# Optimization experiments

Hardware: AMD Instinct MI355X
Metric: run time of the kernel (lower is better)

## Reference

```python
import jax, jax.numpy as jnp
import numpy as np

VOCAB, SEQ, D_EMB, D_HID, BATCH = 50257, 256, 256, 512, 16

def setup_inputs() -> dict:
    key = jax.random.key(0)
    ks = jax.random.split(key, 8)
    s_e = 1.0 / np.sqrt(D_EMB)
    s_h = 1.0 / np.sqrt(D_HID)
    return {
        "idx": jax.random.randint(ks[0], (BATCH, SEQ), 0, VOCAB),
        "E":  jax.random.normal(ks[1], (VOCAB, D_EMB), jnp.float32) * 0.02,
        "Wi": jax.random.normal(ks[2], (D_EMB, 4 * D_HID), jnp.float32) * s_e,  # input kernel (no bias in flax LSTMCell)
        "Wh": jax.random.normal(ks[3], (D_HID, 4 * D_HID), jnp.float32) * s_h,  # recurrent kernel
        "bh": jnp.zeros((4 * D_HID,), jnp.float32),                              # recurrent bias
        "Wo": jax.random.normal(ks[4], (D_HID, VOCAB), jnp.float32) * s_h,
        "bo": jnp.zeros((VOCAB,), jnp.float32),
    }

def reference(idx, E, Wi, Wh, bh, Wo, bo):
    B, S = idx.shape
    H = Wh.shape[0]
    x = E[idx]                                   # [B, S, D] embedding gather
    # precompute input contribution for all timesteps: [S, B, 4H]
    xz = jnp.einsum('bsd,dg->sbg', x, Wi)

    def step(carry, xz_t):
        h, c = carry
        z = xz_t + h @ Wh + bh                   # [B, 4H]
        i, f, g, o = jnp.split(z, 4, axis=-1)    # flax gate order: i, f, g, o
        i = jax.nn.sigmoid(i)
        f = jax.nn.sigmoid(f)
        g = jnp.tanh(g)
        o = jax.nn.sigmoid(o)
        c = f * c + i * g
        h = o * jnp.tanh(c)
        return (h, c), h

    h0 = jnp.zeros((B, H), x.dtype)
    c0 = jnp.zeros((B, H), x.dtype)
    _, hs = jax.lax.scan(step, (h0, c0), xz)     # hs: [S, B, H]
    hs = jnp.transpose(hs, (1, 0, 2))            # [B, S, H]
    logits = hs @ Wo + bo                        # [B, S, V]
    return logits
```

## Files before the change

### kernel.cpp

```cpp
#include <hip/hip_runtime.h>
#include <cstdint>


typedef __attribute__((ext_vector_type(8))) short short8;
typedef __attribute__((ext_vector_type(4))) float f32x4;
typedef __attribute__((ext_vector_type(4))) unsigned int u32x4;
typedef __attribute__((ext_vector_type(4))) unsigned short ush4;

#define DEVFN static __device__ __forceinline__

DEVFN unsigned short f2bf(float f) {
    unsigned int u = __float_as_uint(f);
    return (unsigned short)((u + 0x7FFFu + ((u >> 16) & 1u)) >> 16);
}
DEVFN float bf2f(unsigned short h) { return __uint_as_float(((unsigned int)h) << 16); }
DEVFN float sigm(float x) { return 1.0f / (1.0f + __expf(-x)); }
DEVFN float tanh_fast(float x) {
    float e = __expf(-2.0f * fabsf(x));
    float t = (1.0f - e) / (1.0f + e);
    return copysignf(t, x);
}
DEVFN f32x4 fzero() { f32x4 v = {0.f, 0.f, 0.f, 0.f}; return v; }

DEVFN uint32_t ld_flag_mall(const uint32_t* p) {
    uint32_t v;
    asm volatile("global_load_dword %0, %1, off sc0 sc1\n\ts_waitcnt vmcnt(0)"
                 : "=v"(v) : "v"(p) : "memory");
    return v;
}
DEVFN void st_flag_mall(uint32_t* p, uint32_t v) {
    asm volatile("global_store_dword %0, %1, off sc0 sc1" :: "v"(p), "v"(v) : "memory");
}
DEVFN void aload16(u32x4& d, const void* p) {
    asm volatile("global_load_dwordx4 %0, %1, off sc0 sc1" : "=v"(d) : "v"(p));
}

__global__ __launch_bounds__(256) void k0_wot(const float* __restrict__ Wo,
                                              uint32_t* __restrict__ WoTP) {
    __shared__ float tile[32][33];
    const int bx = blockIdx.x;
    const int cb = bx >> 4;
    const int kb = bx & 15;
    const int c0 = cb * 32, k0 = kb * 32;
    const int j = threadIdx.x & 31;
    const int i0 = threadIdx.x >> 5;
    for (int ii = i0; ii < 32; ii += 8) {
        const int c = c0 + j;
        tile[ii][j] = (c < 50257) ? Wo[(size_t)(k0 + ii) * 50257 + c] : 0.0f;
    }
    __syncthreads();
    for (int ii = i0; ii < 32; ii += 8) {
        const float v = tile[j][ii];
        const unsigned short hi = f2bf(v);
        const unsigned short lo = f2bf(v - bf2f(hi));
        WoTP[(size_t)(c0 + ii) * 512 + k0 + j] = (((unsigned int)hi) << 16) | lo;
    }
}

__global__ __launch_bounds__(256) void k0b_whlo(const float* __restrict__ Wh,
                                                uint32_t* __restrict__ WLO) {
    const int tid = blockIdx.x * 256 + threadIdx.x;
    const int lane = tid & 63;
    const int q    = (tid >> 6) & 15;
    const int nt   = (tid >> 10) & 1;
    const int vp   = tid >> 11;
    const int cc   = lane & 15;
    const int gcol = (cc >> 2) * 512 + vp * 8 + nt * 4 + (cc & 3);
    const int kbase = q * 32 + (lane >> 4) * 8;
    u32x4 o;
#pragma unroll
    for (int p = 0; p < 4; ++p) {
        unsigned int pair = 0;
#pragma unroll
        for (int e = 0; e < 2; ++e) {
            const int k = kbase + p * 2 + e;
            const float w = Wh[(size_t)k * 2048 + gcol];
            const unsigned short hi = f2bf(w);
            const unsigned short lo = f2bf(w - bf2f(hi));
            pair |= ((unsigned int)lo) << (e * 16);
        }
        o[p] = pair;
    }
    *(u32x4*)(WLO + (size_t)tid * 4) = o;
}

__global__ __launch_bounds__(256) void k1_xz(const int* __restrict__ idx,
                                             const float* __restrict__ E,
                                             const float* __restrict__ Wi,
                                             unsigned short* __restrict__ xzH) {
    __shared__ float xs[16][256];
    const int s = blockIdx.x;
    const int t = threadIdx.x;
#pragma unroll
    for (int b = 0; b < 16; ++b) {
        const int row = idx[b * 256 + s];
        xs[b][t] = E[(size_t)row * 256 + t];
    }
    __syncthreads();
    for (int half = 0; half < 2; ++half) {
        const int g0 = half * 1024 + t * 4;
        f32x4 acc[16];
#pragma unroll
        for (int b = 0; b < 16; ++b) acc[b] = fzero();
        for (int d = 0; d < 256; ++d) {
            const f32x4 w = *(const f32x4*)&Wi[(size_t)d * 2048 + g0];
#pragma unroll
            for (int b = 0; b < 16; ++b) {
                const float xv = xs[b][d];
                acc[b] += xv * w;
            }
        }
#pragma unroll
        for (int b = 0; b < 16; ++b) {
            ush4 o;
#pragma unroll
            for (int jj = 0; jj < 4; ++jj) o[jj] = f2bf(acc[b][jj]);
            *(ush4*)&xzH[((size_t)s * 16 + b) * 2048 + g0] = o;
        }
    }
}

__global__ __launch_bounds__(256, 1) void k23(const float* __restrict__ Wh,
                                              const float* __restrict__ bh,
                                              const unsigned short* __restrict__ xzH,
                                              const short8* __restrict__ WLO8,
                                              uint32_t* __restrict__ hsP,
                                              const uint32_t* __restrict__ zeroh,
                                              uint32_t* __restrict__ ep,
                                              uint32_t* __restrict__ epC,
                                              const uint32_t* __restrict__ WoTP,
                                              const float* __restrict__ bo,
                                              float* __restrict__ out) {
    __shared__ __align__(16) char smem[131072];
    __shared__ unsigned int sEp;

    const int tid = threadIdx.x;

    if (blockIdx.x < 16) {
        const int blk = blockIdx.x;

        for (int vs = 0; vs < 4; ++vs) {
            const int vp_s = blk * 4 + vs;
            const int l = tid >> 3, seg = tid & 7;
            const int cc = l & 15, nt0 = l >> 4;
            const int gcol = (cc >> 2) * 512 + vp_s * 8 + nt0 * 4 + (cc & 3);
            for (int k8 = seg * 64; k8 < seg * 64 + 64; k8 += 8) {
                short8 v;
#pragma unroll
                for (int i = 0; i < 8; ++i)
                    v[i] = (short)f2bf(Wh[(size_t)(k8 + i) * 2048 + gcol]);
                const int slot = (k8 >> 3) ^ (l & 7);
                *(short8*)(smem + vs * 32768 + l * 1024 + slot * 16) = v;
            }
        }
        if (tid == 0) sEp = 0;
        __syncthreads();

        const int w = tid >> 6;
        const int lane = tid & 63;
        const int vp = blk * 4 + w;
        unsigned short* whhW = (unsigned short*)(smem + w * 32768);
        const int c = lane & 15;
        const int qtr = lane >> 4;

        int gc[2];
        float bh_v[2];
#pragma unroll
        for (int nt = 0; nt < 2; ++nt) {
            gc[nt] = (c >> 2) * 512 + vp * 8 + nt * 4 + (c & 3);
            bh_v[nt] = bh[gc[nt]];
        }
        float cst[2][4];
#pragma unroll
        for (int nt = 0; nt < 2; ++nt)
#pragma unroll
            for (int r = 0; r < 4; ++r) cst[nt][r] = 0.0f;

        float xzv[2][4];
#pragma unroll
        for (int nt = 0; nt < 2; ++nt)
#pragma unroll
            for (int r = 0; r < 4; ++r)
                xzv[nt][r] = bf2f(xzH[(size_t)(qtr * 4 + r) * 2048 + gc[nt]]);

        short8 bz = {0, 0, 0, 0, 0, 0, 0, 0};
        f32x4 bd0 = fzero(), bd1 = fzero();

        for (int t = 0; t < 256; ++t) {
            if (t > 0) {
                const uint32_t tgt = 16u * (uint32_t)t;
                if (w == 0) {
                    while (true) {
                        const uint32_t v = ld_flag_mall(ep);
                        if (v >= tgt) break;
#pragma unroll
                        for (int i = 0; i < 2; ++i) {
                            bd0 = __builtin_amdgcn_mfma_f32_16x16x32_bf16(bz, bz, bd0, 0, 0, 0);
                            bd1 = __builtin_amdgcn_mfma_f32_16x16x32_bf16(bz, bz, bd1, 0, 0, 0);
                        }
                    }
                    if (lane == 0) {
                        __hip_atomic_store(&sEp, (unsigned)t, __ATOMIC_RELAXED,
                                           __HIP_MEMORY_SCOPE_WORKGROUP);
                        if (blk == 0) st_flag_mall(epC, (uint32_t)t);
                    }
                } else {
                    while (__hip_atomic_load(&sEp, __ATOMIC_RELAXED,
                                             __HIP_MEMORY_SCOPE_WORKGROUP) < (unsigned)t) {}
                }
                __builtin_amdgcn_sched_barrier(0);
            }

            const uint32_t* hbase = (t == 0)
                ? (zeroh + (size_t)c * 512)
                : (hsP + ((size_t)(t - 1) * 16 + c) * 512);

            f32x4 acc[2][2];
#pragma unroll
            for (int nt = 0; nt < 2; ++nt) { acc[nt][0] = fzero(); acc[nt][1] = fzero(); }

#pragma unroll
            for (int q = 0; q < 16; ++q) {
                const int kb = q * 32 + qtr * 8;
                const unsigned long long* hb64 = (const unsigned long long*)(hbase + kb);
                unsigned long long d[4];
#pragma unroll
                for (int i = 0; i < 4; ++i)
                    d[i] = __hip_atomic_load(hb64 + i, __ATOMIC_RELAXED,
                                             __HIP_MEMORY_SCOPE_AGENT);
                short8 ahi, alo;
#pragma unroll
                for (int i = 0; i < 4; ++i) {
                    const uint32_t wlo32 = (uint32_t)d[i];
                    const uint32_t whi32 = (uint32_t)(d[i] >> 32);
                    ahi[2 * i]     = (short)(wlo32 >> 16); alo[2 * i]     = (short)(wlo32 & 0xffffu);
                    ahi[2 * i + 1] = (short)(whi32 >> 16); alo[2 * i + 1] = (short)(whi32 & 0xffffu);
                }
#pragma unroll
                for (int nt = 0; nt < 2; ++nt) {
                    const int l = nt * 16 + c;
                    const short8 bhi = *(const short8*)((const char*)whhW + l * 1024 +
                                                        (((q * 4 + qtr) ^ (l & 7)) << 4));
                    const short8 blo = WLO8[(((size_t)vp * 2 + nt) * 16 + q) * 64 + lane];
                    f32x4 a = acc[nt][q & 1];
                    a = __builtin_amdgcn_mfma_f32_16x16x32_bf16(ahi, bhi, a, 0, 0, 0);
                    a = __builtin_amdgcn_mfma_f32_16x16x32_bf16(ahi, blo, a, 0, 0, 0);
                    a = __builtin_amdgcn_mfma_f32_16x16x32_bf16(alo, bhi, a, 0, 0, 0);
                    acc[nt][q & 1] = a;
                }
            }

#pragma unroll
            for (int nt = 0; nt < 2; ++nt) {
                f32x4 z4 = acc[nt][0] + acc[nt][1];
#pragma unroll
                for (int r = 0; r < 4; ++r) z4[r] += xzv[nt][r] + bh_v[nt];
#pragma unroll
                for (int r = 0; r < 4; ++r) {
                    const int sb = (lane & 0x33);
                    const float zi = __shfl(z4[r], sb);
                    const float zf = __shfl(z4[r], sb | 4);
                    const float zg = __shfl(z4[r], sb | 8);
                    const float zo = __shfl(z4[r], sb | 12);
                    const float iv = sigm(zi), fv = sigm(zf);
                    const float gv = tanh_fast(zg), ov = sigm(zo);
                    const float cv = fv * cst[nt][r] + iv * gv;
                    cst[nt][r] = cv;
                    const float hv = ov * tanh_fast(cv);
                    if ((c >> 2) == 0) {
                        const unsigned short hi = f2bf(hv);
                        const unsigned short lo = f2bf(hv - bf2f(hi));
                        const uint32_t packed = (((uint32_t)hi) << 16) | lo;
                        __hip_atomic_store(
                            &hsP[((size_t)t * 16 + qtr * 4 + r) * 512 + vp * 8 + nt * 4 + c],
                            packed, __ATOMIC_RELAXED, __HIP_MEMORY_SCOPE_AGENT);
                    }
                }
            }

            asm volatile("s_waitcnt vmcnt(0)" ::: "memory");
            __syncthreads();
            if (tid == 0)
                __hip_atomic_fetch_add(ep, 1u, __ATOMIC_RELAXED, __HIP_MEMORY_SCOPE_AGENT);

            if (t < 255) {
#pragma unroll
                for (int nt = 0; nt < 2; ++nt)
#pragma unroll
                    for (int r = 0; r < 4; ++r)
                        xzv[nt][r] = bf2f(xzH[((size_t)(t + 1) * 16 + qtr * 4 + r) * 2048 + gc[nt]]);
            }
        }

        if (blk == 0 && tid == 0) {
            while (ld_flag_mall(ep) < 4096u) {}
            st_flag_mall(epC, 256u);
        }
        asm volatile("" :: "v"(bd0), "v"(bd1));
    } else {
        unsigned short (*Ah)[64] = (unsigned short(*)[64])(smem);
        unsigned short (*Al)[64] = (unsigned short(*)[64])(smem + 16384);
        unsigned short (*Bh)[64] = (unsigned short(*)[64])(smem + 32768);
        unsigned short (*Bl)[64] = (unsigned short(*)[64])(smem + 49152);

        const int cid = blockIdx.x - 16;
        const int lane = tid & 63;
        const int wv = tid >> 6;
        const int wr = wv >> 1, wc = wv & 1;
        const int srow = tid >> 1, shalf = tid & 1;

        short8 bz = {0, 0, 0, 0, 0, 0, 0, 0};
        f32x4 bd0 = fzero(), bd1 = fzero(), bd2 = fzero(), bd3 = fzero();

        for (int s0 = 0; s0 < 32; ++s0) {
            const unsigned need = (unsigned)(s0 * 8 + 8);
            while (true) {
                const uint32_t f = ld_flag_mall(epC);
                if (f >= need) break;
#pragma unroll
                for (int i = 0; i < 8; ++i) {
                    bd0 = __builtin_amdgcn_mfma_f32_16x16x32_bf16(bz, bz, bd0, 0, 0, 0);
                    bd1 = __builtin_amdgcn_mfma_f32_16x16x32_bf16(bz, bz, bd1, 0, 0, 0);
                    bd2 = __builtin_amdgcn_mfma_f32_16x16x32_bf16(bz, bz, bd2, 0, 0, 0);
                    bd3 = __builtin_amdgcn_mfma_f32_16x16x32_bf16(bz, bz, bd3, 0, 0, 0);
                }
            }

            for (int vi = 0; vi < 2; ++vi) {
                const int v = cid + vi * 240;
                if (v >= 393) break;

                f32x4 acc[4][4];
#pragma unroll
                for (int i = 0; i < 4; ++i)
#pragma unroll
                    for (int j = 0; j < 4; ++j) acc[i][j] = fzero();

                for (int kb = 0; kb < 8; ++kb) {
                    __syncthreads();
                    const uint32_t* sa = hsP + (size_t)(s0 * 128 + srow) * 512 + kb * 64 + shalf * 32;
                    const uint32_t* sbp = WoTP + (size_t)(v * 128 + srow) * 512 + kb * 64 + shalf * 32;
                    u32x4 av[8], bv[8];
#pragma unroll
                    for (int g = 0; g < 4; ++g) {
                        aload16(av[2 * g], sa + g * 8);
                        aload16(av[2 * g + 1], sa + g * 8 + 4);
                    }
#pragma unroll
                    for (int g = 0; g < 4; ++g) {
                        bv[2 * g]     = *(const u32x4*)(sbp + g * 8);
                        bv[2 * g + 1] = *(const u32x4*)(sbp + g * 8 + 4);
                    }
                    asm volatile("s_waitcnt vmcnt(0)" ::: "memory");
                    __builtin_amdgcn_sched_barrier(0);
#pragma unroll
                    for (int g = 0; g < 4; ++g) {
                        short8 hi, lo;
#pragma unroll
                        for (int i = 0; i < 4; ++i) {
                            hi[i]     = (short)(av[2 * g][i] >> 16);
                            lo[i]     = (short)(av[2 * g][i] & 0xffffu);
                            hi[4 + i] = (short)(av[2 * g + 1][i] >> 16);
                            lo[4 + i] = (short)(av[2 * g + 1][i] & 0xffffu);
                        }
                        const int sw = ((shalf * 4 + g) ^ (srow & 7)) << 4;
                        *(short8*)((char*)Ah + srow * 128 + sw) = hi;
                        *(short8*)((char*)Al + srow * 128 + sw) = lo;
                    }
#pragma unroll
                    for (int g = 0; g < 4; ++g) {
                        short8 hi, lo;
#pragma unroll
                        for (int i = 0; i < 4; ++i) {
                            hi[i]     = (short)(bv[2 * g][i] >> 16);
                            lo[i]     = (short)(bv[2 * g][i] & 0xffffu);
                            hi[4 + i] = (short)(bv[2 * g + 1][i] >> 16);
                            lo[4 + i] = (short)(bv[2 * g + 1][i] & 0xffffu);
                        }
                        const int sw = ((shalf * 4 + g) ^ (srow & 7)) << 4;
                        *(short8*)((char*)Bh + srow * 128 + sw) = hi;
                        *(short8*)((char*)Bl + srow * 128 + sw) = lo;
                    }
                    __syncthreads();

#pragma unroll
                    for (int q = 0; q < 2; ++q) {
                        short8 afh[4], afl[4], bfh[4], bfl[4];
#pragma unroll
                        for (int mi = 0; mi < 4; ++mi) {
                            const int r = wr * 64 + mi * 16 + (lane & 15);
                            const int sw = ((q * 4 + (lane >> 4)) ^ (r & 7)) << 4;
                            afh[mi] = *(const short8*)((const char*)Ah + r * 128 + sw);
                            afl[mi] = *(const short8*)((const char*)Al + r * 128 + sw);
                        }
#pragma unroll
                        for (int nj = 0; nj < 4; ++nj) {
                            const int r = wc * 64 + nj * 16 + (lane & 15);
                            const int sw = ((q * 4 + (lane >> 4)) ^ (r & 7)) << 4;
                            bfh[nj] = *(const short8*)((const char*)Bh + r * 128 + sw);
                            bfl[nj] = *(const short8*)((const char*)Bl + r * 128 + sw);
                        }
#pragma unroll
                        for (int mi = 0; mi < 4; ++mi)
#pragma unroll
                            for (int nj = 0; nj < 4; ++nj) {
                                f32x4 a = acc[mi][nj];
                                a = __builtin_amdgcn_mfma_f32_16x16x32_bf16(afh[mi], bfh[nj], a, 0, 0, 0);
                                a = __builtin_amdgcn_mfma_f32_16x16x32_bf16(afh[mi], bfl[nj], a, 0, 0, 0);
                                a = __builtin_amdgcn_mfma_f32_16x16x32_bf16(afl[mi], bfh[nj], a, 0, 0, 0);
                                acc[mi][nj] = a;
                            }
                    }
                }

#pragma unroll
                for (int nj = 0; nj < 4; ++nj) {
                    const int colg = v * 128 + wc * 64 + nj * 16 + (lane & 15);
                    if (colg < 50257) {
                        const float bov = bo[colg];
#pragma unroll
                        for (int mi = 0; mi < 4; ++mi)
#pragma unroll
                            for (int r = 0; r < 4; ++r) {
                                const int tr = wr * 64 + mi * 16 + (lane >> 4) * 4 + r;
                                const int ss = s0 * 8 + (tr >> 4);
                                const int bb = tr & 15;
                                out[((size_t)bb * 256 + ss) * 50257 + colg] = acc[mi][nj][r] + bov;
                            }
                    }
                }
            }
        }
        asm volatile("" :: "v"(bd0), "v"(bd1), "v"(bd2), "v"(bd3));
    }
}

#define XZH_OFF   0ull
#define HSP_OFF   16777216ull
#define ZEROH_OFF 25165824ull
#define FLG_OFF   25198592ull
#define WLO_OFF   25198848ull
#define WOT_OFF   27296000ull

extern "C" void kernel_launch(void* const* d_in, const int* in_sizes, int n_in,
                              void* d_out, int out_size, void* d_ws, size_t ws_size,
                              hipStream_t stream) {
    (void)in_sizes; (void)n_in; (void)out_size; (void)ws_size;
    const int*   idx = (const int*)  d_in[0];
    const float* E   = (const float*)d_in[1];
    const float* Wi  = (const float*)d_in[2];
    const float* Wh  = (const float*)d_in[3];
    const float* bh  = (const float*)d_in[4];
    const float* Wo  = (const float*)d_in[5];
    const float* bo  = (const float*)d_in[6];
    float* out = (float*)d_out;
    char* ws = (char*)d_ws;

    unsigned short* xzH   = (unsigned short*)(ws + XZH_OFF);
    uint32_t*       hsP   = (uint32_t*)      (ws + HSP_OFF);
    uint32_t*       zeroh = (uint32_t*)      (ws + ZEROH_OFF);
    uint32_t*       ep    = (uint32_t*)      (ws + FLG_OFF);
    uint32_t*       epC   = (uint32_t*)      (ws + FLG_OFF + 128);
    uint32_t*       WLO   = (uint32_t*)      (ws + WLO_OFF);
    uint32_t*       WoTP  = (uint32_t*)      (ws + WOT_OFF);

    hipMemsetAsync(ws + ZEROH_OFF, 0, 33024, stream);

    hipLaunchKernelGGL(k0_wot,   dim3(25152), dim3(256), 0, stream, Wo, WoTP);
    hipLaunchKernelGGL(k0b_whlo, dim3(512),   dim3(256), 0, stream, Wh, WLO);
    hipLaunchKernelGGL(k1_xz,    dim3(256),   dim3(256), 0, stream, idx, E, Wi, xzH);
    hipLaunchKernelGGL(k23,      dim3(256),   dim3(256), 0, stream,
                       Wh, bh, xzH, (const short8*)WLO, hsP, zeroh, ep, epC, WoTP, bo, out);
}
```

Baseline: 3.347 ms.

## Stage recurrent h in LDS per step and stream prepacked Wh hi fragments

Each recurrent block now cooperatively loads the previous step's packed hidden state (all 16 batch rows) into swizzled LDS with wide loads, then reads MFMA A-fragments from LDS instead of every wave issuing atomic 64-bit global loads. Wh hi bf16 fragments are precomputed by a prep kernel and read from global alongside the lo fragments, which frees LDS for h and removes the in-kernel Wh conversion. The per-block spin is simplified so all waves poll the global flag, replacing the wave-0 plus LDS-flag scheme, with a __syncthreads per step added. This trades per-step global atomic traffic for a block barrier and extra global reads of Wh hi.

New measurement: 3.578 ms. +6.9%, slower.

```diff
diff --git a/kernel.cpp b/kernel.cpp
--- a/kernel.cpp
+++ b/kernel.cpp
@@ -57,8 +57,9 @@
     }
 }
 
-__global__ __launch_bounds__(256) void k0b_whlo(const float* __restrict__ Wh,
-                                                uint32_t* __restrict__ WLO) {
+__global__ __launch_bounds__(256) void k0b_whfrag(const float* __restrict__ Wh,
+                                                  uint32_t* __restrict__ WHI,
+                                                  uint32_t* __restrict__ WLO) {
     const int tid = blockIdx.x * 256 + threadIdx.x;
     const int lane = tid & 63;
     const int q    = (tid >> 6) & 15;
@@ -67,21 +68,23 @@
     const int cc   = lane & 15;
     const int gcol = (cc >> 2) * 512 + vp * 8 + nt * 4 + (cc & 3);
     const int kbase = q * 32 + (lane >> 4) * 8;
-    u32x4 o;
+    u32x4 ohi, olo;
 #pragma unroll
     for (int p = 0; p < 4; ++p) {
-        unsigned int pair = 0;
+        unsigned int phi = 0, plo = 0;
 #pragma unroll
         for (int e = 0; e < 2; ++e) {
             const int k = kbase + p * 2 + e;
             const float w = Wh[(size_t)k * 2048 + gcol];
             const unsigned short hi = f2bf(w);
             const unsigned short lo = f2bf(w - bf2f(hi));
-            pair |= ((unsigned int)lo) << (e * 16);
-        }
-        o[p] = pair;
-    }
-    *(u32x4*)(WLO + (size_t)tid * 4) = o;
+            phi |= ((unsigned int)hi) << (e * 16);
+            plo |= ((unsigned int)lo) << (e * 16);
+        }
+        ohi[p] = phi; olo[p] = plo;
+    }
+    *(u32x4*)(WHI + (size_t)tid * 4) = ohi;
+    *(u32x4*)(WLO + (size_t)tid * 4) = olo;
 }
 
 __global__ __launch_bounds__(256) void k1_xz(const int* __restrict__ idx,
@@ -120,46 +123,25 @@
     }
 }
 
-__global__ __launch_bounds__(256, 1) void k23(const float* __restrict__ Wh,
-                                              const float* __restrict__ bh,
+__global__ __launch_bounds__(256, 1) void k23(const float* __restrict__ bh,
                                               const unsigned short* __restrict__ xzH,
+                                              const short8* __restrict__ WHI8,
                                               const short8* __restrict__ WLO8,
                                               uint32_t* __restrict__ hsP,
-                                              const uint32_t* __restrict__ zeroh,
                                               uint32_t* __restrict__ ep,
                                               uint32_t* __restrict__ epC,
                                               const uint32_t* __restrict__ WoTP,
                                               const float* __restrict__ bo,
                                               float* __restrict__ out) {
     __shared__ __align__(16) char smem[131072];
-    __shared__ unsigned int sEp;
 
     const int tid = threadIdx.x;
 
     if (blockIdx.x < 16) {
         const int blk = blockIdx.x;
-
-        for (int vs = 0; vs < 4; ++vs) {
-            const int vp_s = blk * 4 + vs;
-            const int l = tid >> 3, seg = tid & 7;
-            const int cc = l & 15, nt0 = l >> 4;
-            const int gcol = (cc >> 2) * 512 + vp_s * 8 + nt0 * 4 + (cc & 3);
-            for (int k8 = seg * 64; k8 < seg * 64 + 64; k8 += 8) {
-                short8 v;
-#pragma unroll
-                for (int i = 0; i < 8; ++i)
-                    v[i] = (short)f2bf(Wh[(size_t)(k8 + i) * 2048 + gcol]);
-                const int slot = (k8 >> 3) ^ (l & 7);
-                *(short8*)(smem + vs * 32768 + l * 1024 + slot * 16) = v;
-            }
-        }
-        if (tid == 0) sEp = 0;
-        __syncthreads();
-
         const int w = tid >> 6;
         const int lane = tid & 63;
         const int vp = blk * 4 + w;
-        unsigned short* whhW = (unsigned short*)(smem + w * 32768);
         const int c = lane & 15;
         const int qtr = lane >> 4;
 
@@ -189,31 +171,45 @@
         for (int t = 0; t < 256; ++t) {
             if (t > 0) {
                 const uint32_t tgt = 16u * (uint32_t)t;
-                if (w == 0) {
-                    while (true) {
-                        const uint32_t v = ld_flag_mall(ep);
-                        if (v >= tgt) break;
-#pragma unroll
-                        for (int i = 0; i < 2; ++i) {
-                            bd0 = __builtin_amdgcn_mfma_f32_16x16x32_bf16(bz, bz, bd0, 0, 0, 0);
-                            bd1 = __builtin_amdgcn_mfma_f32_16x16x32_bf16(bz, bz, bd1, 0, 0, 0);
-                        }
-                    }
-                    if (lane == 0) {
-                        __hip_atomic_store(&sEp, (unsigned)t, __ATOMIC_RELAXED,
-                                           __HIP_MEMORY_SCOPE_WORKGROUP);
-                        if (blk == 0) st_flag_mall(epC, (uint32_t)t);
-                    }
-                } else {
-                    while (__hip_atomic_load(&sEp, __ATOMIC_RELAXED,
-                                             __HIP_MEMORY_SCOPE_WORKGROUP) < (unsigned)t) {}
-                }
+                while (true) {
+                    const uint32_t v = ld_flag_mall(ep);
+                    if (v >= tgt) break;
+#pragma unroll
+                    for (int i = 0; i < 2; ++i) {
+                        bd0 = __builtin_amdgcn_mfma_f32_16x16x32_bf16(bz, bz, bd0, 0, 0, 0);
+                        bd1 = __builtin_amdgcn_mfma_f32_16x16x32_bf16(bz, bz, bd1, 0, 0, 0);
+                    }
+                }
+                if (blk == 0 && tid == 0) st_flag_mall(epC, (uint32_t)t);
                 __builtin_amdgcn_sched_barrier(0);
             }
 
-            const uint32_t* hbase = (t == 0)
-                ? (zeroh + (size_t)c * 512)
-                : (hsP + ((size_t)(t - 1) * 16 + c) * 512);
+            if (t == 0) {
+                const u32x4 z = {0u, 0u, 0u, 0u};
+#pragma unroll
+                for (int j = 0; j < 8; ++j) {
+                    const int U = j * 256 + tid;
+                    const int b = U >> 7, u = U & 127;
+                    *(u32x4*)(smem + b * 2048 + ((u ^ (b & 7)) << 4)) = z;
+                }
+            } else {
+                u32x4 gv[8];
+#pragma unroll
+                for (int j = 0; j < 8; ++j) {
+                    const int U = j * 256 + tid;
+                    const int b = U >> 7, u = U & 127;
+                    aload16(gv[j], hsP + ((size_t)(t - 1) * 16 + b) * 512 + u * 4);
+                }
+                asm volatile("s_waitcnt vmcnt(0)" ::: "memory");
+                __builtin_amdgcn_sched_barrier(0);
+#pragma unroll
+                for (int j = 0; j < 8; ++j) {
+                    const int U = j * 256 + tid;
+                    const int b = U >> 7, u = U & 127;
+                    *(u32x4*)(smem + b * 2048 + ((u ^ (b & 7)) << 4)) = gv[j];
+                }
+            }
+            __syncthreads();
 
             f32x4 acc[2][2];
 #pragma unroll
@@ -221,26 +217,18 @@
 
 #pragma unroll
             for (int q = 0; q < 16; ++q) {
-                const int kb = q * 32 + qtr * 8;
-                const unsigned long long* hb64 = (const unsigned long long*)(hbase + kb);
-                unsigned long long d[4];
-#pragma unroll
-                for (int i = 0; i < 4; ++i)
-                    d[i] = __hip_atomic_load(hb64 + i, __ATOMIC_RELAXED,
-                                             __HIP_MEMORY_SCOPE_AGENT);
+                const int u0 = q * 8 + qtr * 2;
+                const u32x4 h0 = *(const u32x4*)(smem + c * 2048 + ((u0 ^ (c & 7)) << 4));
+                const u32x4 h1 = *(const u32x4*)(smem + c * 2048 + (((u0 + 1) ^ (c & 7)) << 4));
                 short8 ahi, alo;
 #pragma unroll
                 for (int i = 0; i < 4; ++i) {
-                    const uint32_t wlo32 = (uint32_t)d[i];
-                    const uint32_t whi32 = (uint32_t)(d[i] >> 32);
-                    ahi[2 * i]     = (short)(wlo32 >> 16); alo[2 * i]     = (short)(wlo32 & 0xffffu);
-                    ahi[2 * i + 1] = (short)(whi32 >> 16); alo[2 * i + 1] = (short)(whi32 & 0xffffu);
+                    ahi[i]     = (short)(h0[i] >> 16); alo[i]     = (short)(h0[i] & 0xffffu);
+                    ahi[4 + i] = (short)(h1[i] >> 16); alo[4 + i] = (short)(h1[i] & 0xffffu);
                 }
 #pragma unroll
                 for (int nt = 0; nt < 2; ++nt) {
-                    const int l = nt * 16 + c;
-                    const short8 bhi = *(const short8*)((const char*)whhW + l * 1024 +
-                                                        (((q * 4 + qtr) ^ (l & 7)) << 4));
+                    const short8 bhi = WHI8[(((size_t)vp * 2 + nt) * 16 + q) * 64 + lane];
                     const short8 blo = WLO8[(((size_t)vp * 2 + nt) * 16 + q) * 64 + lane];
                     f32x4 a = acc[nt][q & 1];
                     a = __builtin_amdgcn_mfma_f32_16x16x32_bf16(ahi, bhi, a, 0, 0, 0);
@@ -437,10 +425,10 @@
 
 #define XZH_OFF   0ull
 #define HSP_OFF   16777216ull
-#define ZEROH_OFF 25165824ull
-#define FLG_OFF   25198592ull
-#define WLO_OFF   25198848ull
-#define WOT_OFF   27296000ull
+#define FLG_OFF   25165824ull
+#define WHI_OFF   25166080ull
+#define WLO_OFF   27263232ull
+#define WOT_OFF   29360384ull
 
 extern "C" void kernel_launch(void* const* d_in, const int* in_sizes, int n_in,
                               void* d_out, int out_size, void* d_ws, size_t ws_size,
@@ -456,19 +444,20 @@
     float* out = (float*)d_out;
     char* ws = (char*)d_ws;
 
-    unsigned short* xzH   = (unsigned short*)(ws + XZH_OFF);
-    uint32_t*       hsP   = (uint32_t*)      (ws + HSP_OFF);
-    uint32_t*       zeroh = (uint32_t*)      (ws + ZEROH_OFF);
-    uint32_t*       ep    = (uint32_t*)      (ws + FLG_OFF);
-    uint32_t*       epC   = (uint32_t*)      (ws + FLG_OFF + 128);
-    uint32_t*       WLO   = (uint32_t*)      (ws + WLO_OFF);
-    uint32_t*       WoTP  = (uint32_t*)      (ws + WOT_OFF);
-
-    hipMemsetAsync(ws + ZEROH_OFF, 0, 33024, stream);
-
-    hipLaunchKernelGGL(k0_wot,   dim3(25152), dim3(256), 0, stream, Wo, WoTP);
-    hipLaunchKernelGGL(k0b_whlo, dim3(512),   dim3(256), 0, stream, Wh, WLO);
-    hipLaunchKernelGGL(k1_xz,    dim3(256),   dim3(256), 0, stream, idx, E, Wi, xzH);
-    hipLaunchKernelGGL(k23,      dim3(256),   dim3(256), 0, stream,
-                       Wh, bh, xzH, (const short8*)WLO, hsP, zeroh, ep, epC, WoTP, bo, out);
-}
+    unsigned short* xzH  = (unsigned short*)(ws + XZH_OFF);
+    uint32_t*       hsP  = (uint32_t*)      (ws + HSP_OFF);
+    uint32_t*       ep   = (uint32_t*)      (ws + FLG_OFF);
+    uint32_t*       epC  = (uint32_t*)      (ws + FLG_OFF + 128);
+    uint32_t*       WHI  = (uint32_t*)      (ws + WHI_OFF);
+    uint32_t*       WLO  = (uint32_t*)      (ws + WLO_OFF);
+    uint32_t*       WoTP = (uint32_t*)      (ws + WOT_OFF);
+
+    hipMemsetAsync(ws + FLG_OFF, 0, 256, stream);
+
+    hipLaunchKernelGGL(k0_wot,    dim3(25152), dim3(256), 0, stream, Wo, WoTP);
+    hipLaunchKernelGGL(k0b_whfrag,dim3(512),   dim3(256), 0, stream, Wh, WHI, WLO);
+    hipLaunchKernelGGL(k1_xz,     dim3(256),   dim3(256), 0, stream, idx, E, Wi, xzH);
+    hipLaunchKernelGGL(k23,       dim3(256),   dim3(256), 0, stream,
+                       bh, xzH, (const short8*)WHI, (const short8*)WLO, hsP, ep, epC,
+                       WoTP, bo, out);
+}
```

## Use arrive/release barrier and staged vector stores for LSTM hidden state

Applied to the files above, without the earlier changes.

The grid-wide per-step barrier is restructured. Instead of wave 0 polling a shared counter and relaying through LDS, the last block to arrive publishes a release flag that every wave polls directly. The release also advances the consumer progress flag each step, which removes the final wait loop. Hidden-state outputs are staged in LDS and written as coalesced 16-byte stores instead of scattered 4-byte atomic stores. This cuts per-step barrier latency and store count, at the cost of an extra __syncthreads and more waves polling global memory.

Result: no change. 3.384 ms (+1.1%).

```diff
diff --git a/kernel.cpp b/kernel.cpp
--- a/kernel.cpp
+++ b/kernel.cpp
@@ -33,6 +33,9 @@
 }
 DEVFN void aload16(u32x4& d, const void* p) {
     asm volatile("global_load_dwordx4 %0, %1, off sc0 sc1" : "=v"(d) : "v"(p));
+}
+DEVFN void astore16(uint32_t* p, u32x4 v) {
+    asm volatile("global_store_dwordx4 %0, %1, off sc0 sc1" :: "v"(p), "v"(v) : "memory");
 }
 
 __global__ __launch_bounds__(256) void k0_wot(const float* __restrict__ Wo,
@@ -126,13 +129,14 @@
                                               const short8* __restrict__ WLO8,
                                               uint32_t* __restrict__ hsP,
                                               const uint32_t* __restrict__ zeroh,
-                                              uint32_t* __restrict__ ep,
+                                              uint32_t* __restrict__ arrive,
+                                              uint32_t* __restrict__ rel,
                                               uint32_t* __restrict__ epC,
                                               const uint32_t* __restrict__ WoTP,
                                               const float* __restrict__ bo,
                                               float* __restrict__ out) {
     __shared__ __align__(16) char smem[131072];
-    __shared__ unsigned int sEp;
+    __shared__ __align__(16) uint32_t hstage[16][32];
 
     const int tid = threadIdx.x;
 
@@ -153,7 +157,6 @@
                 *(short8*)(smem + vs * 32768 + l * 1024 + slot * 16) = v;
             }
         }
-        if (tid == 0) sEp = 0;
         __syncthreads();
 
         const int w = tid >> 6;
@@ -188,25 +191,14 @@
 
         for (int t = 0; t < 256; ++t) {
             if (t > 0) {
-                const uint32_t tgt = 16u * (uint32_t)t;
-                if (w == 0) {
-                    while (true) {
-                        const uint32_t v = ld_flag_mall(ep);
-                        if (v >= tgt) break;
-#pragma unroll
-                        for (int i = 0; i < 2; ++i) {
-                            bd0 = __builtin_amdgcn_mfma_f32_16x16x32_bf16(bz, bz, bd0, 0, 0, 0);
-                            bd1 = __builtin_amdgcn_mfma_f32_16x16x32_bf16(bz, bz, bd1, 0, 0, 0);
-                        }
-                    }
-                    if (lane == 0) {
-                        __hip_atomic_store(&sEp, (unsigned)t, __ATOMIC_RELAXED,
-                                           __HIP_MEMORY_SCOPE_WORKGROUP);
-                        if (blk == 0) st_flag_mall(epC, (uint32_t)t);
-                    }
-                } else {
-                    while (__hip_atomic_load(&sEp, __ATOMIC_RELAXED,
-                                             __HIP_MEMORY_SCOPE_WORKGROUP) < (unsigned)t) {}
+                while (true) {
+                    const uint32_t v = ld_flag_mall(rel);
+                    if (v >= (uint32_t)t) break;
+#pragma unroll
+                    for (int i = 0; i < 2; ++i) {
+                        bd0 = __builtin_amdgcn_mfma_f32_16x16x32_bf16(bz, bz, bd0, 0, 0, 0);
+                        bd1 = __builtin_amdgcn_mfma_f32_16x16x32_bf16(bz, bz, bd1, 0, 0, 0);
+                    }
                 }
                 __builtin_amdgcn_sched_barrier(0);
             }
@@ -270,18 +262,29 @@
                     if ((c >> 2) == 0) {
                         const unsigned short hi = f2bf(hv);
                         const unsigned short lo = f2bf(hv - bf2f(hi));
-                        const uint32_t packed = (((uint32_t)hi) << 16) | lo;
-                        __hip_atomic_store(
-                            &hsP[((size_t)t * 16 + qtr * 4 + r) * 512 + vp * 8 + nt * 4 + c],
-                            packed, __ATOMIC_RELAXED, __HIP_MEMORY_SCOPE_AGENT);
-                    }
-                }
-            }
-
+                        hstage[qtr * 4 + r][w * 8 + nt * 4 + c] =
+                            (((uint32_t)hi) << 16) | lo;
+                    }
+                }
+            }
+
+            __syncthreads();
+            if (tid < 128) {
+                const int b = tid >> 3, ch = tid & 7;
+                const u32x4 val = *(const u32x4*)&hstage[b][ch * 4];
+                astore16(hsP + ((size_t)t * 16 + b) * 512 + blk * 32 + ch * 4, val);
+            }
             asm volatile("s_waitcnt vmcnt(0)" ::: "memory");
             __syncthreads();
-            if (tid == 0)
-                __hip_atomic_fetch_add(ep, 1u, __ATOMIC_RELAXED, __HIP_MEMORY_SCOPE_AGENT);
+
+            if (tid == 0) {
+                const uint32_t old = __hip_atomic_fetch_add(arrive, 1u, __ATOMIC_RELAXED,
+                                                            __HIP_MEMORY_SCOPE_AGENT);
+                if (old == 16u * (uint32_t)(t + 1) - 1u) {
+                    st_flag_mall(rel, (uint32_t)(t + 1));
+                    st_flag_mall(epC, (uint32_t)(t + 1));
+                }
+            }
 
             if (t < 255) {
 #pragma unroll
@@ -290,11 +293,6 @@
                     for (int r = 0; r < 4; ++r)
                         xzv[nt][r] = bf2f(xzH[((size_t)(t + 1) * 16 + qtr * 4 + r) * 2048 + gc[nt]]);
             }
-        }
-
-        if (blk == 0 && tid == 0) {
-            while (ld_flag_mall(ep) < 4096u) {}
-            st_flag_mall(epC, 256u);
         }
         asm volatile("" :: "v"(bd0), "v"(bd1));
     } else {
@@ -439,8 +437,8 @@
 #define HSP_OFF   16777216ull
 #define ZEROH_OFF 25165824ull
 #define FLG_OFF   25198592ull
-#define WLO_OFF   25198848ull
-#define WOT_OFF   27296000ull
+#define WLO_OFF   25199360ull
+#define WOT_OFF   27296512ull
 
 extern "C" void kernel_launch(void* const* d_in, const int* in_sizes, int n_in,
                               void* d_out, int out_size, void* d_ws, size_t ws_size,
@@ -456,19 +454,21 @@
     float* out = (float*)d_out;
     char* ws = (char*)d_ws;
 
-    unsigned short* xzH   = (unsigned short*)(ws + XZH_OFF);
-    uint32_t*       hsP   = (uint32_t*)      (ws + HSP_OFF);
-    uint32_t*       zeroh = (uint32_t*)      (ws + ZEROH_OFF);
-    uint32_t*       ep    = (uint32_t*)      (ws + FLG_OFF);
-    uint32_t*       epC   = (uint32_t*)      (ws + FLG_OFF + 128);
-    uint32_t*       WLO   = (uint32_t*)      (ws + WLO_OFF);
-    uint32_t*       WoTP  = (uint32_t*)      (ws + WOT_OFF);
-
-    hipMemsetAsync(ws + ZEROH_OFF, 0, 33024, stream);
+    unsigned short* xzH    = (unsigned short*)(ws + XZH_OFF);
+    uint32_t*       hsP    = (uint32_t*)      (ws + HSP_OFF);
+    uint32_t*       zeroh  = (uint32_t*)      (ws + ZEROH_OFF);
+    uint32_t*       arrive = (uint32_t*)      (ws + FLG_OFF);
+    uint32_t*       rel    = (uint32_t*)      (ws + FLG_OFF + 128);
+    uint32_t*       epC    = (uint32_t*)      (ws + FLG_OFF + 256);
+    uint32_t*       WLO    = (uint32_t*)      (ws + WLO_OFF);
+    uint32_t*       WoTP   = (uint32_t*)      (ws + WOT_OFF);
+
+    hipMemsetAsync(ws + ZEROH_OFF, 0, 33536, stream);
 
     hipLaunchKernelGGL(k0_wot,   dim3(25152), dim3(256), 0, stream, Wo, WoTP);
     hipLaunchKernelGGL(k0b_whlo, dim3(512),   dim3(256), 0, stream, Wh, WLO);
     hipLaunchKernelGGL(k1_xz,    dim3(256),   dim3(256), 0, stream, idx, E, Wi, xzH);
     hipLaunchKernelGGL(k23,      dim3(256),   dim3(256), 0, stream,
-                       Wh, bh, xzH, (const short8*)WLO, hsP, zeroh, ep, epC, WoTP, bo, out);
-}
+                       Wh, bh, xzH, (const short8*)WLO, hsP, zeroh, arrive, rel, epC,
+                       WoTP, bo, out);
+}
```

## Replace shared counter barrier with per-wave step flags polled wave-wide

Applied to the files above, without the earlier changes.

Drops the single atomic counter plus the workgroup-level relay through LDS and the second consumer flag. Instead, each of the 64 recurrent waves publishes its own step flag, and every wave polls all 64 flags with one lane per flag, combined through a wave vote. The per-block __syncthreads before signalling goes away, so waves advance independently. The loads of the previous hidden state are also batched into 32 outstanding 16-byte cache-bypassing loads before any MFMA work, which raises memory-level parallelism. The risks are more polling traffic, because every wave reads 64 flags, and the ordering now relies on a waitcnt before a relaxed flag store. The flags memset is not visible, so initialisation to zero is assumed.

Measured after the change: 4.221 ms. 1.26x slower.

```diff
diff --git a/kernel.cpp b/kernel.cpp
--- a/kernel.cpp
+++ b/kernel.cpp
@@ -22,15 +22,6 @@
 }
 DEVFN f32x4 fzero() { f32x4 v = {0.f, 0.f, 0.f, 0.f}; return v; }
 
-DEVFN uint32_t ld_flag_mall(const uint32_t* p) {
-    uint32_t v;
-    asm volatile("global_load_dword %0, %1, off sc0 sc1\n\ts_waitcnt vmcnt(0)"
-                 : "=v"(v) : "v"(p) : "memory");
-    return v;
-}
-DEVFN void st_flag_mall(uint32_t* p, uint32_t v) {
-    asm volatile("global_store_dword %0, %1, off sc0 sc1" :: "v"(p), "v"(v) : "memory");
-}
 DEVFN void aload16(u32x4& d, const void* p) {
     asm volatile("global_load_dwordx4 %0, %1, off sc0 sc1" : "=v"(d) : "v"(p));
 }
@@ -126,13 +117,11 @@
                                               const short8* __restrict__ WLO8,
                                               uint32_t* __restrict__ hsP,
                                               const uint32_t* __restrict__ zeroh,
-                                              uint32_t* __restrict__ ep,
-                                              uint32_t* __restrict__ epC,
+                                              uint32_t* __restrict__ flags,
                                               const uint32_t* __restrict__ WoTP,
                                               const float* __restrict__ bo,
                                               float* __restrict__ out) {
     __shared__ __align__(16) char smem[131072];
-    __shared__ unsigned int sEp;
 
     const int tid = threadIdx.x;
 
@@ -153,7 +142,6 @@
                 *(short8*)(smem + vs * 32768 + l * 1024 + slot * 16) = v;
             }
         }
-        if (tid == 0) sEp = 0;
         __syncthreads();
 
         const int w = tid >> 6;
@@ -188,25 +176,15 @@
 
         for (int t = 0; t < 256; ++t) {
             if (t > 0) {
-                const uint32_t tgt = 16u * (uint32_t)t;
-                if (w == 0) {
-                    while (true) {
-                        const uint32_t v = ld_flag_mall(ep);
-                        if (v >= tgt) break;
-#pragma unroll
-                        for (int i = 0; i < 2; ++i) {
-                            bd0 = __builtin_amdgcn_mfma_f32_16x16x32_bf16(bz, bz, bd0, 0, 0, 0);
-                            bd1 = __builtin_amdgcn_mfma_f32_16x16x32_bf16(bz, bz, bd1, 0, 0, 0);
-                        }
-                    }
-                    if (lane == 0) {
-                        __hip_atomic_store(&sEp, (unsigned)t, __ATOMIC_RELAXED,
-                                           __HIP_MEMORY_SCOPE_WORKGROUP);
-                        if (blk == 0) st_flag_mall(epC, (uint32_t)t);
-                    }
-                } else {
-                    while (__hip_atomic_load(&sEp, __ATOMIC_RELAXED,
-                                             __HIP_MEMORY_SCOPE_WORKGROUP) < (unsigned)t) {}
+                while (true) {
+                    const uint32_t v = __hip_atomic_load(flags + lane, __ATOMIC_RELAXED,
+                                                         __HIP_MEMORY_SCOPE_AGENT);
+                    if (__all((int)(v >= (uint32_t)t))) break;
+#pragma unroll
+                    for (int i = 0; i < 2; ++i) {
+                        bd0 = __builtin_amdgcn_mfma_f32_16x16x32_bf16(bz, bz, bd0, 0, 0, 0);
+                        bd1 = __builtin_amdgcn_mfma_f32_16x16x32_bf16(bz, bz, bd1, 0, 0, 0);
+                    }
                 }
                 __builtin_amdgcn_sched_barrier(0);
             }
@@ -215,26 +193,29 @@
                 ? (zeroh + (size_t)c * 512)
                 : (hsP + ((size_t)(t - 1) * 16 + c) * 512);
 
-            f32x4 acc[2][2];
-#pragma unroll
-            for (int nt = 0; nt < 2; ++nt) { acc[nt][0] = fzero(); acc[nt][1] = fzero(); }
-
+            u32x4 hb[32];
 #pragma unroll
             for (int q = 0; q < 16; ++q) {
                 const int kb = q * 32 + qtr * 8;
-                const unsigned long long* hb64 = (const unsigned long long*)(hbase + kb);
-                unsigned long long d[4];
-#pragma unroll
-                for (int i = 0; i < 4; ++i)
-                    d[i] = __hip_atomic_load(hb64 + i, __ATOMIC_RELAXED,
-                                             __HIP_MEMORY_SCOPE_AGENT);
+                aload16(hb[2 * q],     hbase + kb);
+                aload16(hb[2 * q + 1], hbase + kb + 4);
+            }
+            asm volatile("s_waitcnt vmcnt(0)" ::: "memory");
+            __builtin_amdgcn_sched_barrier(0);
+
+            f32x4 acc[2][2];
+#pragma unroll
+            for (int nt = 0; nt < 2; ++nt) { acc[nt][0] = fzero(); acc[nt][1] = fzero(); }
+
+#pragma unroll
+            for (int q = 0; q < 16; ++q) {
                 short8 ahi, alo;
 #pragma unroll
                 for (int i = 0; i < 4; ++i) {
-                    const uint32_t wlo32 = (uint32_t)d[i];
-                    const uint32_t whi32 = (uint32_t)(d[i] >> 32);
-                    ahi[2 * i]     = (short)(wlo32 >> 16); alo[2 * i]     = (short)(wlo32 & 0xffffu);
-                    ahi[2 * i + 1] = (short)(whi32 >> 16); alo[2 * i + 1] = (short)(whi32 & 0xffffu);
+                    ahi[i]     = (short)(hb[2 * q][i] >> 16);
+                    alo[i]     = (short)(hb[2 * q][i] & 0xffffu);
+                    ahi[4 + i] = (short)(hb[2 * q + 1][i] >> 16);
+                    alo[4 + i] = (short)(hb[2 * q + 1][i] & 0xffffu);
                 }
 #pragma unroll
                 for (int nt = 0; nt < 2; ++nt) {
@@ -279,9 +260,9 @@
             }
 
             asm volatile("s_waitcnt vmcnt(0)" ::: "memory");
-            __syncthreads();
-            if (tid == 0)
-                __hip_atomic_fetch_add(ep, 1u, __ATOMIC_RELAXED, __HIP_MEMORY_SCOPE_AGENT);
+            if (lane == 0)
+                __hip_atomic_store(&flags[vp], (uint32_t)(t + 1), __ATOMIC_RELAXED,
+                                   __HIP_MEMORY_SCOPE_AGENT);
 
             if (t < 255) {
 #pragma unroll
@@ -290,11 +271,6 @@
                     for (int r = 0; r < 4; ++r)
                         xzv[nt][r] = bf2f(xzH[((size_t)(t + 1) * 16 + qtr * 4 + r) * 2048 + gc[nt]]);
             }
-        }
-
-        if (blk == 0 && tid == 0) {
-            while (ld_flag_mall(ep) < 4096u) {}
-            st_flag_mall(epC, 256u);
         }
         asm volatile("" :: "v"(bd0), "v"(bd1));
     } else {
@@ -315,8 +291,9 @@
         for (int s0 = 0; s0 < 32; ++s0) {
             const unsigned need = (unsigned)(s0 * 8 + 8);
             while (true) {
-                const uint32_t f = ld_flag_mall(epC);
-                if (f >= need) break;
+                const uint32_t f = __hip_atomic_load(flags + lane, __ATOMIC_RELAXED,
+                                                     __HIP_MEMORY_SCOPE_AGENT);
+                if (__all((int)(f >= need))) break;
 #pragma unroll
                 for (int i = 0; i < 8; ++i) {
                     bd0 = __builtin_amdgcn_mfma_f32_16x16x32_bf16(bz, bz, bd0, 0, 0, 0);
@@ -459,8 +436,7 @@
     unsigned short* xzH   = (unsigned short*)(ws + XZH_OFF);
     uint32_t*       hsP   = (uint32_t*)      (ws + HSP_OFF);
     uint32_t*       zeroh = (uint32_t*)      (ws + ZEROH_OFF);
-    uint32_t*       ep    = (uint32_t*)      (ws + FLG_OFF);
-    uint32_t*       epC   = (uint32_t*)      (ws + FLG_OFF + 128);
+    uint32_t*       flags = (uint32_t*)      (ws + FLG_OFF);
     uint32_t*       WLO   = (uint32_t*)      (ws + WLO_OFF);
     uint32_t*       WoTP  = (uint32_t*)      (ws + WOT_OFF);
 
@@ -470,5 +446,5 @@
     hipLaunchKernelGGL(k0b_whlo, dim3(512),   dim3(256), 0, stream, Wh, WLO);
     hipLaunchKernelGGL(k1_xz,    dim3(256),   dim3(256), 0, stream, idx, E, Wi, xzH);
     hipLaunchKernelGGL(k23,      dim3(256),   dim3(256), 0, stream,
-                       Wh, bh, xzH, (const short8*)WLO, hsP, zeroh, ep, epC, WoTP, bo, out);
-}
+                       Wh, bh, xzH, (const short8*)WLO, hsP, zeroh, flags, WoTP, bo, out);
+}
```
